# Kernel optimization log

Hardware: AMD Instinct MI355X
Metric: run time of the kernel (lower is better)

## Reference

```python
import jax, jax.numpy as jnp
import numpy as np

L = 6          # number of GNN layers
D = 128        # feature_dim (d_model)
H = 4          # num_heads (hardcoded in AttentionalPropagation)
DH = D // H    # per-head dim
N = 2048       # number of segments/keypoints per frame
B = 1          # batch
NAMES = ["self", "cross"] * (L // 2)
EPS = 1e-5     # InstanceNorm1d eps


def _conv1(W, b, x):
    # Conv1d kernel_size=1: W [out,in], x [b,in,n] -> [b,out,n]
    return jnp.einsum('oi,bin->bon', W, x) + b[None, :, None]


def _inorm(x):
    # InstanceNorm1d (affine=False): normalize over the length axis per (batch, channel)
    m = jnp.mean(x, axis=-1, keepdims=True)
    v = jnp.mean((x - m) ** 2, axis=-1, keepdims=True)
    return (x - m) * jax.lax.rsqrt(v + EPS)


def _attn_block(x, src, p):
    Wq, bq, Wk, bk, Wv, bv, Wm, bm, W1, b1, W2, b2 = p
    b_dim, _, n = x.shape
    # view(b, dim, heads, -1): channel axis split as (DH, H)
    q = _conv1(Wq, bq, x).reshape(b_dim, DH, H, -1)
    k = _conv1(Wk, bk, src).reshape(b_dim, DH, H, -1)
    v = _conv1(Wv, bv, src).reshape(b_dim, DH, H, -1)
    scores = jnp.einsum('bdhn,bdhm->bhnm', q, k) / jnp.sqrt(jnp.asarray(DH, x.dtype))
    prob = jax.nn.softmax(scores, axis=-1)
    msg = jnp.einsum('bhnm,bdhm->bdhn', prob, v).reshape(b_dim, D, -1)
    msg = _conv1(Wm, bm, msg)
    # MLP([2D, 2D, D]): Conv1d -> InstanceNorm1d -> ReLU -> Conv1d
    h = _conv1(W1, b1, jnp.concatenate([x, msg], axis=1))
    h = jax.nn.relu(_inorm(h))
    return _conv1(W2, b2, h)


def setup_inputs() -> dict:
    key = jax.random.key(0)
    ks = jax.random.split(key, 14)
    s = 0.05
    f32 = jnp.float32
    return {
        "desc0": jax.random.normal(ks[0], (B, D, N), f32),
        "desc1": jax.random.normal(ks[1], (B, D, N), f32),
        "Wq": jax.random.normal(ks[2], (L, D, D), f32) * s,
        "bq": jnp.zeros((L, D), f32),
        "Wk": jax.random.normal(ks[3], (L, D, D), f32) * s,
        "bk": jnp.zeros((L, D), f32),
        "Wv": jax.random.normal(ks[4], (L, D, D), f32) * s,
        "bv": jnp.zeros((L, D), f32),
        "Wm": jax.random.normal(ks[5], (L, D, D), f32) * s,
        "bm": jnp.zeros((L, D), f32),
        "W1": jax.random.normal(ks[6], (L, 2 * D, 2 * D), f32) * s,
        "b1": jnp.zeros((L, 2 * D), f32),
        "W2": jax.random.normal(ks[7], (L, D, 2 * D), f32) * s,
        "b2": jnp.zeros((L, D), f32),  # nn.init.constant_(mlp[-1].bias, 0.0)
    }


def reference(desc0, desc1, Wq, bq, Wk, bk, Wv, bv, Wm, bm, W1, b1, W2, b2):
    params = (Wq, bq, Wk, bk, Wv, bv, Wm, bm, W1, b1, W2, b2)
    for l in range(L):
        p = tuple(a[l] for a in params)
        if NAMES[l] == 'cross':
            src0, src1 = desc1, desc0
        else:
            src0, src1 = desc0, desc1
        delta0 = _attn_block(desc0, src0, p)
        delta1 = _attn_block(desc1, src1, p)
        desc0 = desc0 + delta0
        desc1 = desc1 + delta1
    return desc0, desc1
```

## Files before the change

kernel.cpp:

```cpp
#include <hip/hip_runtime.h>

#define NN 2048
#define DDIM 128
#define NHEAD 4
#define DH 32
#define NL 6

typedef __attribute__((ext_vector_type(8))) __bf16 bf16x8;
typedef __attribute__((ext_vector_type(4))) float f32x4;

__device__ __forceinline__ unsigned int f2bf(float x) {
  unsigned int u = __float_as_uint(x);
  u += 0x7fff + ((u >> 16) & 1);
  return u >> 16;
}
__device__ __forceinline__ unsigned int pk2(float a, float b) {
  return f2bf(a) | (f2bf(b) << 16);
}
__device__ __forceinline__ float bf2f(unsigned short u) {
  return __uint_as_float(((unsigned int)u) << 16);
}

__global__ __launch_bounds__(256) void setup_kernel(
    const float* __restrict__ Wq, const float* __restrict__ Wk,
    const float* __restrict__ Wv, const float* __restrict__ Wm,
    const float* __restrict__ W1, const float* __restrict__ W2,
    const float* __restrict__ bmv, const float* __restrict__ b1,
    const float* __restrict__ desc0, const float* __restrict__ desc1,
    unsigned short* __restrict__ Wqkv, unsigned short* __restrict__ Wb2,
    unsigned short* __restrict__ Wmix, float* __restrict__ b1m,
    unsigned short* __restrict__ dT0, unsigned short* __restrict__ dT1,
    float* __restrict__ o0, float* __restrict__ o1,
    float* __restrict__ SgAll) {
  __shared__ __align__(16) unsigned char ARENA[17408];
  const int bid = blockIdx.x;
  const int t = threadIdx.x;

  if (bid < 672) {
    int idx = (bid * 256 + t) * 4;
    if (idx >= 688128) return;
    const float* src; unsigned short* dst; int soff, doff;
    if (idx < 98304)       { src = Wq; soff = idx; dst = Wqkv; doff = idx; }
    else if (idx < 196608) { src = Wk; soff = idx - 98304; dst = Wqkv; doff = idx; }
    else if (idx < 294912) { src = Wv; soff = idx - 196608; dst = Wqkv; doff = idx; }
    else if (idx < 491520) { src = W2; soff = idx - 294912; dst = Wb2; doff = soff; }
    else {
      int f = idx - 491520;
      int l = f >> 15, rem = f & 32767;
      int i = rem >> 7, c = rem & 127;
      src = W1; soff = (l << 16) + (i << 8) + c;
      dst = Wmix; doff = (l << 16) + (i << 8) + c;
    }
    float4 v = *(const float4*)&src[soff];
    uint2 p = { pk2(v.x, v.y), pk2(v.z, v.w) };
    *(uint2*)&dst[doff] = p;
  } else if (bid < 720) {
    const int b = bid - 672;
    const int jb = b & 1, ib = (b >> 1) & 3, l = b >> 3;
    const int bj = jb * 64, bi = ib * 64;
    float* Ws = (float*)ARENA;
    float* Xs = (float*)ARENA + 2080;
    const int ti = (t >> 4) << 2;
    const int tj = (t & 15) << 2;
    float acc[4][4] = {{0.f}};
    for (int k0 = 0; k0 < 128; k0 += 32) {
#pragma unroll
      for (int i = 0; i < 8; ++i) {
        int e = t + i * 256;
        int ii = e >> 5, kk = e & 31;
        Ws[kk * 65 + ii] = W1[(size_t)(l << 16) + (bi + ii) * 256 + 128 + k0 + kk];
      }
#pragma unroll
      for (int i = 0; i < 2; ++i) {
        int e = t + i * 256;
        int r = e >> 4, c4 = e & 15;
        *(float4*)&Xs[r * 64 + c4 * 4] =
            *(const float4*)&Wm[(size_t)l * 16384 + (k0 + r) * 128 + bj + c4 * 4];
      }
      __syncthreads();
#pragma unroll
      for (int kk = 0; kk < 32; ++kk) {
        float a[4];
        a[0] = Ws[kk * 65 + ti]; a[1] = Ws[kk * 65 + ti + 1];
        a[2] = Ws[kk * 65 + ti + 2]; a[3] = Ws[kk * 65 + ti + 3];
        float4 b4 = *(const float4*)&Xs[kk * 64 + tj];
        float bb[4] = {b4.x, b4.y, b4.z, b4.w};
#pragma unroll
        for (int i = 0; i < 4; ++i)
#pragma unroll
          for (int j = 0; j < 4; ++j) acc[i][j] += a[i] * bb[j];
      }
      __syncthreads();
    }
#pragma unroll
    for (int i = 0; i < 4; ++i) {
      uint2 p = { pk2(acc[i][0], acc[i][1]), pk2(acc[i][2], acc[i][3]) };
      *(uint2*)&Wmix[(size_t)(l << 16) + (bi + ti + i) * 256 + 128 + bj + tj] = p;
    }
    if (jb == 0 && ib == 0) {
      float a = b1[l * 256 + t];
      const float* wr = &W1[(size_t)(l << 16) + t * 256 + 128];
      const float* bp = &bmv[l * 128];
      for (int k = 0; k < 128; k += 4)
        a += wr[k] * bp[k] + wr[k + 1] * bp[k + 1] + wr[k + 2] * bp[k + 2] + wr[k + 3] * bp[k + 3];
      b1m[l * 256 + t] = a;
    }
  } else if (bid < 784) {
    const int b = bid - 720;
    const float* D = (b >> 5) ? desc1 : desc0;
    unsigned short* T = (b >> 5) ? dT1 : dT0;
    float* O = (b >> 5) ? o1 : o0;
    const int n0 = (b & 31) * 64;
    unsigned short* L = (unsigned short*)ARENA;
#pragma unroll
    for (int i = 0; i < 8; ++i) {
      int idx = t + i * 256;
      int c = idx >> 4, nj = (idx & 15) * 4;
      float4 v = *(const float4*)&D[(size_t)c * NN + n0 + nj];
      *(float4*)&O[(size_t)c * NN + n0 + nj] = v;
      L[(nj + 0) * 136 + c] = (unsigned short)f2bf(v.x);
      L[(nj + 1) * 136 + c] = (unsigned short)f2bf(v.y);
      L[(nj + 2) * 136 + c] = (unsigned short)f2bf(v.z);
      L[(nj + 3) * 136 + c] = (unsigned short)f2bf(v.w);
    }
    __syncthreads();
#pragma unroll
    for (int i = 0; i < 4; ++i) {
      int idx = t + i * 256;
      int n = idx >> 4, cj = (idx & 15) * 8;
      uint4 v = *(const uint4*)&L[n * 136 + cj];
      *(uint4*)&T[(size_t)(n0 + n) * 128 + cj] = v;
    }
  } else {
    float4 z = make_float4(0.f, 0.f, 0.f, 0.f);
    *(float4*)&SgAll[(bid - 784) * 1024 + t * 4] = z;
  }
}

struct MOp {
  const unsigned short* A;
  const float* bias;
  const unsigned short* B1;
  const unsigned short* B2;
  unsigned short* Cb;
  float* Cf;
  const float* Sp;
  int ldb, ldc, mode;
};
struct MOps8 { MOp op[8]; };

template <int K>
__global__ __launch_bounds__(256) void gemm_direct_kernel(MOps8 P) {
  const MOp g = P.op[blockIdx.z];
  const int t = threadIdx.x;
  const int w = t >> 6, lane = t & 63;
  const int col = lane & 15, Qd = lane >> 4;
  const int bm = blockIdx.y * 64;
  const int bn = blockIdx.x * 64;

  __shared__ float meanL[256], rstdL[256];
  __shared__ float swS[4][64], swQ[4][64];

  if (g.mode == 4) {
    float s = g.Sp[t * 2], ss = g.Sp[t * 2 + 1];
    float mean = s * (1.0f / NN);
    float var = fmaxf(ss * (1.0f / NN) - mean * mean, 0.f);
    meanL[t] = mean;
    rstdL[t] = rsqrtf(var + 1e-5f);
  }
  __syncthreads();

  const int n = bn + w * 16 + col;
  f32x4 acc[4];
#pragma unroll
  for (int mt = 0; mt < 4; ++mt) acc[mt] = (f32x4){0.f, 0.f, 0.f, 0.f};

#pragma unroll
  for (int k0 = 0; k0 < K; k0 += 32) {
    bf16x8 af[4];
#pragma unroll
    for (int mt = 0; mt < 4; ++mt)
      af[mt] = *(const bf16x8*)&g.A[(size_t)(bm + mt * 16 + col) * K + k0 + Qd * 8];
    const unsigned short* Bp = g.B1;
    int kk = k0;
    if (g.B2 && k0 >= 128) { Bp = g.B2; kk = k0 - 128; }
    uint4 v = *(const uint4*)&Bp[(size_t)n * g.ldb + kk + Qd * 8];
    if (g.mode == 4) {
      float4 mA = *(const float4*)&meanL[k0 + Qd * 8];
      float4 mB = *(const float4*)&meanL[k0 + Qd * 8 + 4];
      float4 rA = *(const float4*)&rstdL[k0 + Qd * 8];
      float4 rB = *(const float4*)&rstdL[k0 + Qd * 8 + 4];
      union { uint4 q; unsigned short us[8]; } u;
      u.q = v;
      float x0 = fmaxf((bf2f(u.us[0]) - mA.x) * rA.x, 0.f);
      float x1 = fmaxf((bf2f(u.us[1]) - mA.y) * rA.y, 0.f);
      float x2 = fmaxf((bf2f(u.us[2]) - mA.z) * rA.z, 0.f);
      float x3 = fmaxf((bf2f(u.us[3]) - mA.w) * rA.w, 0.f);
      float x4 = fmaxf((bf2f(u.us[4]) - mB.x) * rB.x, 0.f);
      float x5 = fmaxf((bf2f(u.us[5]) - mB.y) * rB.y, 0.f);
      float x6 = fmaxf((bf2f(u.us[6]) - mB.z) * rB.z, 0.f);
      float x7 = fmaxf((bf2f(u.us[7]) - mB.w) * rB.w, 0.f);
      u.q.x = pk2(x0, x1); u.q.y = pk2(x2, x3);
      u.q.z = pk2(x4, x5); u.q.w = pk2(x6, x7);
      v = u.q;
    }
    union { uint4 q; bf16x8 b; } bc;
    bc.q = v;
#pragma unroll
    for (int mt = 0; mt < 4; ++mt)
      acc[mt] = __builtin_amdgcn_mfma_f32_16x16x32_bf16(af[mt], bc.b, acc[mt], 0, 0, 0);
  }

#pragma unroll
  for (int mt = 0; mt < 4; ++mt) {
    const int c0 = bm + mt * 16 + Qd * 4;
    const float b0 = g.bias[c0], b1 = g.bias[c0 + 1];
    const float b2 = g.bias[c0 + 2], b3 = g.bias[c0 + 3];
    f32x4 a = acc[mt];
    float v0 = a[0] + b0, v1 = a[1] + b1, v2 = a[2] + b2, v3 = a[3] + b3;
    if (g.mode <= 2) {
      if (g.mode == 0) {
        const float sc = 0.25503488f;
        v0 *= sc; v1 *= sc; v2 *= sc; v3 *= sc;
      }
      const int d = c0 >> 2;
      if (g.mode == 1) {
        g.Cb[((size_t)0 * NN + n) * 32 + d] = (unsigned short)f2bf(v0);
        g.Cb[((size_t)1 * NN + n) * 32 + d] = (unsigned short)f2bf(v1);
        g.Cb[((size_t)2 * NN + n) * 32 + d] = (unsigned short)f2bf(v2);
        g.Cb[((size_t)3 * NN + n) * 32 + d] = (unsigned short)f2bf(v3);
      } else {
        g.Cb[(size_t)(0 * 32 + d) * NN + n] = (unsigned short)f2bf(v0);
        g.Cb[(size_t)(1 * 32 + d) * NN + n] = (unsigned short)f2bf(v1);
        g.Cb[(size_t)(2 * 32 + d) * NN + n] = (unsigned short)f2bf(v2);
        g.Cb[(size_t)(3 * 32 + d) * NN + n] = (unsigned short)f2bf(v3);
      }
    } else if (g.mode == 5) {
      uint2 pv = { pk2(v0, v1), pk2(v2, v3) };
      *(uint2*)&g.Cb[(size_t)n * g.ldc + c0] = pv;
      float sA[4] = {v0, v1, v2, v3};
      float sQ[4] = {v0 * v0, v1 * v1, v2 * v2, v3 * v3};
#pragma unroll
      for (int r = 0; r < 4; ++r) {
#pragma unroll
        for (int off = 1; off < 16; off <<= 1) {
          sA[r] += __shfl_xor(sA[r], off);
          sQ[r] += __shfl_xor(sQ[r], off);
        }
      }
      if (col == 0) {
#pragma unroll
        for (int r = 0; r < 4; ++r) {
          swS[w][mt * 16 + Qd * 4 + r] = sA[r];
          swQ[w][mt * 16 + Qd * 4 + r] = sQ[r];
        }
      }
    } else {
      float* dp = g.Cf;
      float o0 = dp[(size_t)(c0 + 0) * NN + n] + v0;
      float o1 = dp[(size_t)(c0 + 1) * NN + n] + v1;
      float o2 = dp[(size_t)(c0 + 2) * NN + n] + v2;
      float o3 = dp[(size_t)(c0 + 3) * NN + n] + v3;
      dp[(size_t)(c0 + 0) * NN + n] = o0;
      dp[(size_t)(c0 + 1) * NN + n] = o1;
      dp[(size_t)(c0 + 2) * NN + n] = o2;
      dp[(size_t)(c0 + 3) * NN + n] = o3;
      uint2 pv = { pk2(o0, o1), pk2(o2, o3) };
      *(uint2*)&g.Cb[(size_t)n * g.ldc + c0] = pv;
    }
  }
  if (g.mode == 5) {
    __syncthreads();
    if (t < 64) {
      float a = swS[0][t] + swS[1][t] + swS[2][t] + swS[3][t];
      float b = swQ[0][t] + swQ[1][t] + swQ[2][t] + swQ[3][t];
      atomicAdd(&g.Cf[(bm + t) * 2], a);
      atomicAdd(&g.Cf[(bm + t) * 2 + 1], b);
    }
  }
}

struct FDesc {
  const unsigned short* HT; const float* Sp; float* outF; unsigned short* dT;
  unsigned short* Qb; unsigned short* Kt; unsigned short* Vb;
};
struct FArgs {
  FDesc d[2];
  const unsigned short *W2l, *Wql, *Wkl, *Wvl;
  const float *b2l, *bql, *bkl, *bvl;
};

__global__ __launch_bounds__(256) void fused_tail_kernel(FArgs F) {
  const FDesc g = F.d[blockIdx.y];
  const int t = threadIdx.x;
  const int w = t >> 6, lane = t & 63;
  const int col = lane & 15, Qd = lane >> 4;
  const int nb = blockIdx.x * 16;
  const int n = nb + col;

  __shared__ float meanL[256], rstdL[256];
  __shared__ __align__(16) unsigned short dTs[16 * 136];

  {
    float s = g.Sp[t * 2], ss = g.Sp[t * 2 + 1];
    float mean = s * (1.0f / NN);
    float var = fmaxf(ss * (1.0f / NN) - mean * mean, 0.f);
    meanL[t] = mean;
    rstdL[t] = rsqrtf(var + 1e-5f);
  }
  __syncthreads();

  f32x4 accA[2];
  accA[0] = (f32x4){0.f, 0.f, 0.f, 0.f};
  accA[1] = (f32x4){0.f, 0.f, 0.f, 0.f};
#pragma unroll
  for (int k0 = 0; k0 < 256; k0 += 32) {
    uint4 v = *(const uint4*)&g.HT[(size_t)n * 256 + k0 + Qd * 8];
    float4 mA = *(const float4*)&meanL[k0 + Qd * 8];
    float4 mB = *(const float4*)&meanL[k0 + Qd * 8 + 4];
    float4 rA = *(const float4*)&rstdL[k0 + Qd * 8];
    float4 rB = *(const float4*)&rstdL[k0 + Qd * 8 + 4];
    union { uint4 q; unsigned short us[8]; } u;
    u.q = v;
    float x0 = fmaxf((bf2f(u.us[0]) - mA.x) * rA.x, 0.f);
    float x1 = fmaxf((bf2f(u.us[1]) - mA.y) * rA.y, 0.f);
    float x2 = fmaxf((bf2f(u.us[2]) - mA.z) * rA.z, 0.f);
    float x3 = fmaxf((bf2f(u.us[3]) - mA.w) * rA.w, 0.f);
    float x4 = fmaxf((bf2f(u.us[4]) - mB.x) * rB.x, 0.f);
    float x5 = fmaxf((bf2f(u.us[5]) - mB.y) * rB.y, 0.f);
    float x6 = fmaxf((bf2f(u.us[6]) - mB.z) * rB.z, 0.f);
    float x7 = fmaxf((bf2f(u.us[7]) - mB.w) * rB.w, 0.f);
    u.q.x = pk2(x0, x1); u.q.y = pk2(x2, x3);
    u.q.z = pk2(x4, x5); u.q.w = pk2(x6, x7);
    union { uint4 q; bf16x8 b; } bc;
    bc.q = u.q;
#pragma unroll
    for (int mt = 0; mt < 2; ++mt) {
      bf16x8 af = *(const bf16x8*)&F.W2l[(size_t)(w * 32 + mt * 16 + col) * 256 + k0 + Qd * 8];
      accA[mt] = __builtin_amdgcn_mfma_f32_16x16x32_bf16(af, bc.b, accA[mt], 0, 0, 0);
    }
  }
#pragma unroll
  for (int mt = 0; mt < 2; ++mt) {
    const int c0 = w * 32 + mt * 16 + Qd * 4;
    f32x4 a = accA[mt];
    float o0 = g.outF[(size_t)(c0 + 0) * NN + n] + a[0] + F.b2l[c0 + 0];
    float o1 = g.outF[(size_t)(c0 + 1) * NN + n] + a[1] + F.b2l[c0 + 1];
    float o2 = g.outF[(size_t)(c0 + 2) * NN + n] + a[2] + F.b2l[c0 + 2];
    float o3 = g.outF[(size_t)(c0 + 3) * NN + n] + a[3] + F.b2l[c0 + 3];
    g.outF[(size_t)(c0 + 0) * NN + n] = o0;
    g.outF[(size_t)(c0 + 1) * NN + n] = o1;
    g.outF[(size_t)(c0 + 2) * NN + n] = o2;
    g.outF[(size_t)(c0 + 3) * NN + n] = o3;
    unsigned short s0 = (unsigned short)f2bf(o0), s1 = (unsigned short)f2bf(o1);
    unsigned short s2 = (unsigned short)f2bf(o2), s3 = (unsigned short)f2bf(o3);
    dTs[col * 136 + c0 + 0] = s0;
    dTs[col * 136 + c0 + 1] = s1;
    dTs[col * 136 + c0 + 2] = s2;
    dTs[col * 136 + c0 + 3] = s3;
    uint2 pv = { ((unsigned int)s0) | (((unsigned int)s1) << 16),
                 ((unsigned int)s2) | (((unsigned int)s3) << 16) };
    *(uint2*)&g.dT[(size_t)n * 128 + c0] = pv;
  }
  __syncthreads();

  f32x4 accB[6];
#pragma unroll
  for (int f = 0; f < 6; ++f) accB[f] = (f32x4){0.f, 0.f, 0.f, 0.f};
#pragma unroll
  for (int k0 = 0; k0 < 128; k0 += 32) {
    bf16x8 bq = *(const bf16x8*)&dTs[col * 136 + k0 + Qd * 8];
#pragma unroll
    for (int f = 0; f < 6; ++f) {
      const int idx = w * 6 + f;
      const int op = idx >> 3, mt = idx & 7;
      const unsigned short* W = (op == 0) ? F.Wql : (op == 1) ? F.Wkl : F.Wvl;
      bf16x8 af = *(const bf16x8*)&W[(size_t)(mt * 16 + col) * 128 + k0 + Qd * 8];
      accB[f] = __builtin_amdgcn_mfma_f32_16x16x32_bf16(af, bq, accB[f], 0, 0, 0);
    }
  }
#pragma unroll
  for (int f = 0; f < 6; ++f) {
    const int idx = w * 6 + f;
    const int op = idx >> 3, mt = idx & 7;
    const float* bias = (op == 0) ? F.bql : (op == 1) ? F.bkl : F.bvl;
    const int c0 = mt * 16 + Qd * 4;
    f32x4 a = accB[f];
    float v0 = a[0] + bias[c0], v1 = a[1] + bias[c0 + 1];
    float v2 = a[2] + bias[c0 + 2], v3 = a[3] + bias[c0 + 3];
    const int d = c0 >> 2;
    if (op == 0) {
      const float sc = 0.25503488f;
      v0 *= sc; v1 *= sc; v2 *= sc; v3 *= sc;
      g.Qb[(size_t)(0 * 32 + d) * NN + n] = (unsigned short)f2bf(v0);
      g.Qb[(size_t)(1 * 32 + d) * NN + n] = (unsigned short)f2bf(v1);
      g.Qb[(size_t)(2 * 32 + d) * NN + n] = (unsigned short)f2bf(v2);
      g.Qb[(size_t)(3 * 32 + d) * NN + n] = (unsigned short)f2bf(v3);
    } else if (op == 1) {
      g.Kt[((size_t)0 * NN + n) * 32 + d] = (unsigned short)f2bf(v0);
      g.Kt[((size_t)1 * NN + n) * 32 + d] = (unsigned short)f2bf(v1);
      g.Kt[((size_t)2 * NN + n) * 32 + d] = (unsigned short)f2bf(v2);
      g.Kt[((size_t)3 * NN + n) * 32 + d] = (unsigned short)f2bf(v3);
    } else {
      g.Vb[(size_t)(0 * 32 + d) * NN + n] = (unsigned short)f2bf(v0);
      g.Vb[(size_t)(1 * 32 + d) * NN + n] = (unsigned short)f2bf(v1);
      g.Vb[(size_t)(2 * 32 + d) * NN + n] = (unsigned short)f2bf(v2);
      g.Vb[(size_t)(3 * 32 + d) * NN + n] = (unsigned short)f2bf(v3);
    }
  }
}

__global__ __launch_bounds__(256, 4) void attn_mfma_kernel(
    const unsigned short* __restrict__ Qb0, const unsigned short* __restrict__ Kt0,
    const unsigned short* __restrict__ Vb0, const unsigned short* __restrict__ Qb1,
    const unsigned short* __restrict__ Kt1, const unsigned short* __restrict__ Vb1,
    unsigned short* __restrict__ mgT0, unsigned short* __restrict__ mgT1, int cross) {
  const int z = blockIdx.y, desc = z >> 2, h = z & 3;
  const int t = threadIdx.x;
  const int wid = t >> 6, lane = t & 63;
  const int col = lane & 15, Qd = lane >> 4;
  const int qb = blockIdx.x * 16;

  const unsigned short* Qb = desc ? Qb1 : Qb0;
  const int s = cross ? (1 - desc) : desc;
  const unsigned short* Kt = s ? Kt1 : Kt0;
  const unsigned short* Vb = s ? Vb1 : Vb0;

  __shared__ __align__(16) unsigned short SM[7424];
  unsigned short* PW = SM + wid * 640;
  float* fS = (float*)(SM + 2560);

  bf16x8 bq;
  {
    union { unsigned short u[8]; bf16x8 v; } tmp;
#pragma unroll
    for (int j = 0; j < 8; ++j)
      tmp.u[j] = Qb[(size_t)(h * 32 + Qd * 8 + j) * NN + qb + col];
    bq = tmp.v;
  }

  f32x4 o0 = {0.f, 0.f, 0.f, 0.f}, o1 = {0.f, 0.f, 0.f, 0.f};
  float m = -1e30f, l = 0.f;

  const int kq = wid * 512;
#pragma unroll 2
  for (int it = 0; it < 16; ++it) {
    const int k0 = kq + it * 32;
    bf16x8 aK0 = *(const bf16x8*)&Kt[((size_t)h * NN + k0 + col) * 32 + Qd * 8];
    bf16x8 aK1 = *(const bf16x8*)&Kt[((size_t)h * NN + k0 + 16 + col) * 32 + Qd * 8];
    bf16x8 av0 = *(const bf16x8*)&Vb[(size_t)(h * 32 + col) * NN + k0 + Qd * 8];
    bf16x8 av1 = *(const bf16x8*)&Vb[(size_t)(h * 32 + 16 + col) * NN + k0 + Qd * 8];
    f32x4 z4 = {0.f, 0.f, 0.f, 0.f};
    f32x4 s0 = __builtin_amdgcn_mfma_f32_16x16x32_bf16(aK0, bq, z4, 0, 0, 0);
    f32x4 s1 = __builtin_amdgcn_mfma_f32_16x16x32_bf16(aK1, bq, z4, 0, 0, 0);
    float cm = fmaxf(fmaxf(fmaxf(s0[0], s0[1]), fmaxf(s0[2], s0[3])),
                     fmaxf(fmaxf(s1[0], s1[1]), fmaxf(s1[2], s1[3])));
    cm = fmaxf(cm, __shfl_xor(cm, 16));
    cm = fmaxf(cm, __shfl_xor(cm, 32));
    const float mn = fmaxf(m, cm);
    const float alpha = exp2f(m - mn);
    m = mn;
    float p00 = exp2f(s0[0] - mn), p01 = exp2f(s0[1] - mn);
    float p02 = exp2f(s0[2] - mn), p03 = exp2f(s0[3] - mn);
    float p10 = exp2f(s1[0] - mn), p11 = exp2f(s1[1] - mn);
    float p12 = exp2f(s1[2] - mn), p13 = exp2f(s1[3] - mn);
    float us = (p00 + p01) + (p02 + p03) + (p10 + p11) + (p12 + p13);
    us += __shfl_xor(us, 16);
    us += __shfl_xor(us, 32);
    l = l * alpha + us;
    uint2 w0 = { pk2(p00, p01), pk2(p02, p03) };
    uint2 w1 = { pk2(p10, p11), pk2(p12, p13) };
    *(uint2*)&PW[col * 40 + Qd * 4] = w0;
    *(uint2*)&PW[col * 40 + 16 + Qd * 4] = w1;
    bf16x8 pb = *(const bf16x8*)&PW[col * 40 + Qd * 8];
    o0 = o0 * alpha;
    o1 = o1 * alpha;
    o0 = __builtin_amdgcn_mfma_f32_16x16x32_bf16(av0, pb, o0, 0, 0, 0);
    o1 = __builtin_amdgcn_mfma_f32_16x16x32_bf16(av1, pb, o1, 0, 0, 0);
  }

  __syncthreads();
  *(float4*)&fS[wid * 576 + col * 36 + Qd * 4] =
      make_float4(o0[0], o0[1], o0[2], o0[3]);
  *(float4*)&fS[wid * 576 + col * 36 + 16 + Qd * 4] =
      make_float4(o1[0], o1[1], o1[2], o1[3]);
  if (Qd == 0) {
    fS[2304 + wid * 16 + col] = m;
    fS[2368 + wid * 16 + col] = l;
  }
  __syncthreads();
  {
    const int q16 = t >> 4, dg = t & 15;
    float m0 = fS[2304 + q16], m1 = fS[2304 + 16 + q16];
    float m2 = fS[2304 + 32 + q16], m3 = fS[2304 + 48 + q16];
    float M = fmaxf(fmaxf(m0, m1), fmaxf(m2, m3));
    float w0 = exp2f(m0 - M), w1 = exp2f(m1 - M);
    float w2 = exp2f(m2 - M), w3 = exp2f(m3 - M);
    float L = w0 * fS[2368 + q16] + w1 * fS[2368 + 16 + q16] +
              w2 * fS[2368 + 32 + q16] + w3 * fS[2368 + 48 + q16];
    float inv = 1.0f / L;
    unsigned short* T = desc ? mgT1 : mgT0;
    const int q = qb + q16;
#pragma unroll
    for (int r = 0; r < 2; ++r) {
      int d = dg * 2 + r;
      float v = (w0 * fS[0 * 576 + q16 * 36 + d] + w1 * fS[1 * 576 + q16 * 36 + d] +
                 w2 * fS[2 * 576 + q16 * 36 + d] + w3 * fS[3 * 576 + q16 * 36 + d]) * inv;
      T[(size_t)q * 128 + d * 4 + h] = (unsigned short)f2bf(v);
    }
  }
}

extern "C" void kernel_launch(void* const* d_in, const int* in_sizes, int n_in,
                              void* d_out, int out_size, void* d_ws, size_t ws_size,
                              hipStream_t stream) {
  const float* desc0 = (const float*)d_in[0];
  const float* desc1 = (const float*)d_in[1];
  const float* Wq = (const float*)d_in[2];
  const float* bq = (const float*)d_in[3];
  const float* Wk = (const float*)d_in[4];
  const float* bk = (const float*)d_in[5];
  const float* Wv = (const float*)d_in[6];
  const float* bv = (const float*)d_in[7];
  const float* Wm = (const float*)d_in[8];
  const float* bmv = (const float*)d_in[9];
  const float* W1 = (const float*)d_in[10];
  const float* b1 = (const float*)d_in[11];
  const float* W2 = (const float*)d_in[12];
  const float* b2 = (const float*)d_in[13];

  float* out0 = (float*)d_out;
  float* out1 = out0 + (size_t)DDIM * NN;

  float* fws = (float*)d_ws;
  float* SgAll = fws;
  float* b1m = SgAll + 6144;
  unsigned short* uws = (unsigned short*)(b1m + 1536);
  unsigned short* dT0 = uws;
  unsigned short* dT1 = uws + 1 * 262144;
  unsigned short* Qb0 = uws + 2 * 262144;
  unsigned short* Qb1 = uws + 3 * 262144;
  unsigned short* Kt0 = uws + 4 * 262144;
  unsigned short* Kt1 = uws + 5 * 262144;
  unsigned short* Vb0 = uws + 6 * 262144;
  unsigned short* Vb1 = uws + 7 * 262144;
  unsigned short* mgT0 = uws + 8 * 262144;
  unsigned short* mgT1 = uws + 9 * 262144;
  unsigned short* HT0 = uws + 10 * 262144;
  unsigned short* HT1 = HT0 + 524288;
  unsigned short* Wqkv = HT1 + 524288;
  unsigned short* Wb2 = Wqkv + 294912;
  unsigned short* Wmix = Wb2 + 196608;

  setup_kernel<<<790, 256, 0, stream>>>(Wq, Wk, Wv, Wm, W1, W2, bmv, b1,
                                        desc0, desc1, Wqkv, Wb2, Wmix, b1m,
                                        dT0, dT1, out0, out1, SgAll);

  {
    MOps8 Pq = {};
    Pq.op[0] = {Wqkv, bq, dT0, nullptr, Qb0, nullptr, nullptr, 128, 0, 0};
    Pq.op[1] = {Wqkv, bq, dT1, nullptr, Qb1, nullptr, nullptr, 128, 0, 0};
    Pq.op[2] = {Wqkv + 98304, bk, dT0, nullptr, Kt0, nullptr, nullptr, 128, 0, 1};
    Pq.op[3] = {Wqkv + 98304, bk, dT1, nullptr, Kt1, nullptr, nullptr, 128, 0, 1};
    Pq.op[4] = {Wqkv + 196608, bv, dT0, nullptr, Vb0, nullptr, nullptr, 128, 0, 2};
    Pq.op[5] = {Wqkv + 196608, bv, dT1, nullptr, Vb1, nullptr, nullptr, 128, 0, 2};
    gemm_direct_kernel<128><<<dim3(32, 2, 6), 256, 0, stream>>>(Pq);
  }

  for (int l = 0; l < NL; ++l) {
    const int cross = l & 1;
    const unsigned short* wmx = Wmix + l * 65536;
    const unsigned short* w2 = Wb2 + l * 32768;
    const float* b1p = b1m + (size_t)l * 256;
    const float* b2p = b2 + (size_t)l * 128;
    float* Sg0 = SgAll + l * 1024;
    float* Sg1 = Sg0 + 512;

    attn_mfma_kernel<<<dim3(128, 8), 256, 0, stream>>>(
        Qb0, Kt0, Vb0, Qb1, Kt1, Vb1, mgT0, mgT1, cross);

    MOps8 P1 = {};
    P1.op[0] = {wmx, b1p, dT0, mgT0, HT0, Sg0, nullptr, 128, 256, 5};
    P1.op[1] = {wmx, b1p, dT1, mgT1, HT1, Sg1, nullptr, 128, 256, 5};
    gemm_direct_kernel<256><<<dim3(32, 4, 2), 256, 0, stream>>>(P1);

    if (l < NL - 1) {
      FArgs F;
      F.d[0] = {HT0, Sg0, out0, dT0, Qb0, Kt0, Vb0};
      F.d[1] = {HT1, Sg1, out1, dT1, Qb1, Kt1, Vb1};
      F.W2l = w2;
      F.Wql = Wqkv + (l + 1) * 16384;
      F.Wkl = Wqkv + 98304 + (l + 1) * 16384;
      F.Wvl = Wqkv + 196608 + (l + 1) * 16384;
      F.b2l = b2p;
      F.bql = bq + (size_t)(l + 1) * 128;
      F.bkl = bk + (size_t)(l + 1) * 128;
      F.bvl = bv + (size_t)(l + 1) * 128;
      fused_tail_kernel<<<dim3(128, 2), 256, 0, stream>>>(F);
    } else {
      MOps8 P2 = {};
      P2.op[0] = {w2, b2p, HT0, nullptr, dT0, out0, Sg0, 256, 128, 4};
      P2.op[1] = {w2, b2p, HT1, nullptr, dT1, out1, Sg1, 256, 128, 4};
      gemm_direct_kernel<256><<<dim3(32, 2, 2), 256, 0, stream>>>(P2);
    }
  }
}
```

Before: 402.7 us.

## Fuse attention and first MLP GEMM via last-arriving-block counter

Merges the attention kernel and the first MLP conv GEMM into one kernel. Each of the four head blocks for a 16-query tile increments a per-tile atomic counter, and the last block to arrive computes the 256-channel MLP1 GEMM for that tile. It then writes HT and accumulates instance-norm statistics with global atomics. This removes one kernel launch per layer and the gap between the two kernels, at the cost of a threadfence, more global atomics, and extra GEMM work on the winning block.

```diff
diff --git a/kernel.cpp b/kernel.cpp
--- a/kernel.cpp
+++ b/kernel.cpp
@@ -31,7 +31,7 @@
     unsigned short* __restrict__ Wmix, float* __restrict__ b1m,
     unsigned short* __restrict__ dT0, unsigned short* __restrict__ dT1,
     float* __restrict__ o0, float* __restrict__ o1,
-    float* __restrict__ SgAll) {
+    float* __restrict__ SgAll, float* __restrict__ cntAll) {
   __shared__ __align__(16) unsigned char ARENA[17408];
   const int bid = blockIdx.x;
   const int t = threadIdx.x;
@@ -132,8 +132,10 @@
       *(uint4*)&T[(size_t)(n0 + n) * 128 + cj] = v;
     }
   } else {
+    const int b = bid - 784;
     float4 z = make_float4(0.f, 0.f, 0.f, 0.f);
-    *(float4*)&SgAll[(bid - 784) * 1024 + t * 4] = z;
+    *(float4*)&SgAll[b * 1024 + t * 4] = z;
+    if (t < 64) *(float4*)&cntAll[b * 256 + t * 4] = z;
   }
 }
 
@@ -159,7 +161,6 @@
   const int bn = blockIdx.x * 64;
 
   __shared__ float meanL[256], rstdL[256];
-  __shared__ float swS[4][64], swQ[4][64];
 
   if (g.mode == 4) {
     float s = g.Sp[t * 2], ss = g.Sp[t * 2 + 1];
@@ -235,26 +236,6 @@
         g.Cb[(size_t)(2 * 32 + d) * NN + n] = (unsigned short)f2bf(v2);
         g.Cb[(size_t)(3 * 32 + d) * NN + n] = (unsigned short)f2bf(v3);
       }
-    } else if (g.mode == 5) {
-      uint2 pv = { pk2(v0, v1), pk2(v2, v3) };
-      *(uint2*)&g.Cb[(size_t)n * g.ldc + c0] = pv;
-      float sA[4] = {v0, v1, v2, v3};
-      float sQ[4] = {v0 * v0, v1 * v1, v2 * v2, v3 * v3};
-#pragma unroll
-      for (int r = 0; r < 4; ++r) {
-#pragma unroll
-        for (int off = 1; off < 16; off <<= 1) {
-          sA[r] += __shfl_xor(sA[r], off);
-          sQ[r] += __shfl_xor(sQ[r], off);
-        }
-      }
-      if (col == 0) {
-#pragma unroll
-        for (int r = 0; r < 4; ++r) {
-          swS[w][mt * 16 + Qd * 4 + r] = sA[r];
-          swQ[w][mt * 16 + Qd * 4 + r] = sQ[r];
-        }
-      }
     } else {
       float* dp = g.Cf;
       float o0 = dp[(size_t)(c0 + 0) * NN + n] + v0;
@@ -269,164 +250,34 @@
       *(uint2*)&g.Cb[(size_t)n * g.ldc + c0] = pv;
     }
   }
-  if (g.mode == 5) {
-    __syncthreads();
-    if (t < 64) {
-      float a = swS[0][t] + swS[1][t] + swS[2][t] + swS[3][t];
-      float b = swQ[0][t] + swQ[1][t] + swQ[2][t] + swQ[3][t];
-      atomicAdd(&g.Cf[(bm + t) * 2], a);
-      atomicAdd(&g.Cf[(bm + t) * 2 + 1], b);
-    }
-  }
-}
-
-struct FDesc {
-  const unsigned short* HT; const float* Sp; float* outF; unsigned short* dT;
-  unsigned short* Qb; unsigned short* Kt; unsigned short* Vb;
+}
+
+struct AArgs {
+  const unsigned short *Qb0, *Kt0, *Vb0, *Qb1, *Kt1, *Vb1;
+  unsigned short *mgT0, *mgT1;
+  const unsigned short *dT0, *dT1;
+  unsigned short *HT0, *HT1;
+  float *Sg0, *Sg1;
+  const unsigned short* Wmx;
+  const float* b1p;
+  int* cnt;
+  int cross;
 };
-struct FArgs {
-  FDesc d[2];
-  const unsigned short *W2l, *Wql, *Wkl, *Wvl;
-  const float *b2l, *bql, *bkl, *bvl;
-};
-
-__global__ __launch_bounds__(256) void fused_tail_kernel(FArgs F) {
-  const FDesc g = F.d[blockIdx.y];
-  const int t = threadIdx.x;
-  const int w = t >> 6, lane = t & 63;
-  const int col = lane & 15, Qd = lane >> 4;
-  const int nb = blockIdx.x * 16;
-  const int n = nb + col;
-
-  __shared__ float meanL[256], rstdL[256];
-  __shared__ __align__(16) unsigned short dTs[16 * 136];
-
-  {
-    float s = g.Sp[t * 2], ss = g.Sp[t * 2 + 1];
-    float mean = s * (1.0f / NN);
-    float var = fmaxf(ss * (1.0f / NN) - mean * mean, 0.f);
-    meanL[t] = mean;
-    rstdL[t] = rsqrtf(var + 1e-5f);
-  }
-  __syncthreads();
-
-  f32x4 accA[2];
-  accA[0] = (f32x4){0.f, 0.f, 0.f, 0.f};
-  accA[1] = (f32x4){0.f, 0.f, 0.f, 0.f};
-#pragma unroll
-  for (int k0 = 0; k0 < 256; k0 += 32) {
-    uint4 v = *(const uint4*)&g.HT[(size_t)n * 256 + k0 + Qd * 8];
-    float4 mA = *(const float4*)&meanL[k0 + Qd * 8];
-    float4 mB = *(const float4*)&meanL[k0 + Qd * 8 + 4];
-    float4 rA = *(const float4*)&rstdL[k0 + Qd * 8];
-    float4 rB = *(const float4*)&rstdL[k0 + Qd * 8 + 4];
-    union { uint4 q; unsigned short us[8]; } u;
-    u.q = v;
-    float x0 = fmaxf((bf2f(u.us[0]) - mA.x) * rA.x, 0.f);
-    float x1 = fmaxf((bf2f(u.us[1]) - mA.y) * rA.y, 0.f);
-    float x2 = fmaxf((bf2f(u.us[2]) - mA.z) * rA.z, 0.f);
-    float x3 = fmaxf((bf2f(u.us[3]) - mA.w) * rA.w, 0.f);
-    float x4 = fmaxf((bf2f(u.us[4]) - mB.x) * rB.x, 0.f);
-    float x5 = fmaxf((bf2f(u.us[5]) - mB.y) * rB.y, 0.f);
-    float x6 = fmaxf((bf2f(u.us[6]) - mB.z) * rB.z, 0.f);
-    float x7 = fmaxf((bf2f(u.us[7]) - mB.w) * rB.w, 0.f);
-    u.q.x = pk2(x0, x1); u.q.y = pk2(x2, x3);
-    u.q.z = pk2(x4, x5); u.q.w = pk2(x6, x7);
-    union { uint4 q; bf16x8 b; } bc;
-    bc.q = u.q;
-#pragma unroll
-    for (int mt = 0; mt < 2; ++mt) {
-      bf16x8 af = *(const bf16x8*)&F.W2l[(size_t)(w * 32 + mt * 16 + col) * 256 + k0 + Qd * 8];
-      accA[mt] = __builtin_amdgcn_mfma_f32_16x16x32_bf16(af, bc.b, accA[mt], 0, 0, 0);
-    }
-  }
-#pragma unroll
-  for (int mt = 0; mt < 2; ++mt) {
-    const int c0 = w * 32 + mt * 16 + Qd * 4;
-    f32x4 a = accA[mt];
-    float o0 = g.outF[(size_t)(c0 + 0) * NN + n] + a[0] + F.b2l[c0 + 0];
-    float o1 = g.outF[(size_t)(c0 + 1) * NN + n] + a[1] + F.b2l[c0 + 1];
-    float o2 = g.outF[(size_t)(c0 + 2) * NN + n] + a[2] + F.b2l[c0 + 2];
-    float o3 = g.outF[(size_t)(c0 + 3) * NN + n] + a[3] + F.b2l[c0 + 3];
-    g.outF[(size_t)(c0 + 0) * NN + n] = o0;
-    g.outF[(size_t)(c0 + 1) * NN + n] = o1;
-    g.outF[(size_t)(c0 + 2) * NN + n] = o2;
-    g.outF[(size_t)(c0 + 3) * NN + n] = o3;
-    unsigned short s0 = (unsigned short)f2bf(o0), s1 = (unsigned short)f2bf(o1);
-    unsigned short s2 = (unsigned short)f2bf(o2), s3 = (unsigned short)f2bf(o3);
-    dTs[col * 136 + c0 + 0] = s0;
-    dTs[col * 136 + c0 + 1] = s1;
-    dTs[col * 136 + c0 + 2] = s2;
-    dTs[col * 136 + c0 + 3] = s3;
-    uint2 pv = { ((unsigned int)s0) | (((unsigned int)s1) << 16),
-                 ((unsigned int)s2) | (((unsigned int)s3) << 16) };
-    *(uint2*)&g.dT[(size_t)n * 128 + c0] = pv;
-  }
-  __syncthreads();
-
-  f32x4 accB[6];
-#pragma unroll
-  for (int f = 0; f < 6; ++f) accB[f] = (f32x4){0.f, 0.f, 0.f, 0.f};
-#pragma unroll
-  for (int k0 = 0; k0 < 128; k0 += 32) {
-    bf16x8 bq = *(const bf16x8*)&dTs[col * 136 + k0 + Qd * 8];
-#pragma unroll
-    for (int f = 0; f < 6; ++f) {
-      const int idx = w * 6 + f;
-      const int op = idx >> 3, mt = idx & 7;
-      const unsigned short* W = (op == 0) ? F.Wql : (op == 1) ? F.Wkl : F.Wvl;
-      bf16x8 af = *(const bf16x8*)&W[(size_t)(mt * 16 + col) * 128 + k0 + Qd * 8];
-      accB[f] = __builtin_amdgcn_mfma_f32_16x16x32_bf16(af, bq, accB[f], 0, 0, 0);
-    }
-  }
-#pragma unroll
-  for (int f = 0; f < 6; ++f) {
-    const int idx = w * 6 + f;
-    const int op = idx >> 3, mt = idx & 7;
-    const float* bias = (op == 0) ? F.bql : (op == 1) ? F.bkl : F.bvl;
-    const int c0 = mt * 16 + Qd * 4;
-    f32x4 a = accB[f];
-    float v0 = a[0] + bias[c0], v1 = a[1] + bias[c0 + 1];
-    float v2 = a[2] + bias[c0 + 2], v3 = a[3] + bias[c0 + 3];
-    const int d = c0 >> 2;
-    if (op == 0) {
-      const float sc = 0.25503488f;
-      v0 *= sc; v1 *= sc; v2 *= sc; v3 *= sc;
-      g.Qb[(size_t)(0 * 32 + d) * NN + n] = (unsigned short)f2bf(v0);
-      g.Qb[(size_t)(1 * 32 + d) * NN + n] = (unsigned short)f2bf(v1);
-      g.Qb[(size_t)(2 * 32 + d) * NN + n] = (unsigned short)f2bf(v2);
-      g.Qb[(size_t)(3 * 32 + d) * NN + n] = (unsigned short)f2bf(v3);
-    } else if (op == 1) {
-      g.Kt[((size_t)0 * NN + n) * 32 + d] = (unsigned short)f2bf(v0);
-      g.Kt[((size_t)1 * NN + n) * 32 + d] = (unsigned short)f2bf(v1);
-      g.Kt[((size_t)2 * NN + n) * 32 + d] = (unsigned short)f2bf(v2);
-      g.Kt[((size_t)3 * NN + n) * 32 + d] = (unsigned short)f2bf(v3);
-    } else {
-      g.Vb[(size_t)(0 * 32 + d) * NN + n] = (unsigned short)f2bf(v0);
-      g.Vb[(size_t)(1 * 32 + d) * NN + n] = (unsigned short)f2bf(v1);
-      g.Vb[(size_t)(2 * 32 + d) * NN + n] = (unsigned short)f2bf(v2);
-      g.Vb[(size_t)(3 * 32 + d) * NN + n] = (unsigned short)f2bf(v3);
-    }
-  }
-}
-
-__global__ __launch_bounds__(256, 4) void attn_mfma_kernel(
-    const unsigned short* __restrict__ Qb0, const unsigned short* __restrict__ Kt0,
-    const unsigned short* __restrict__ Vb0, const unsigned short* __restrict__ Qb1,
-    const unsigned short* __restrict__ Kt1, const unsigned short* __restrict__ Vb1,
-    unsigned short* __restrict__ mgT0, unsigned short* __restrict__ mgT1, int cross) {
+
+__global__ __launch_bounds__(256, 4) void attn_mlp1_kernel(AArgs A) {
   const int z = blockIdx.y, desc = z >> 2, h = z & 3;
   const int t = threadIdx.x;
   const int wid = t >> 6, lane = t & 63;
   const int col = lane & 15, Qd = lane >> 4;
   const int qb = blockIdx.x * 16;
 
-  const unsigned short* Qb = desc ? Qb1 : Qb0;
-  const int s = cross ? (1 - desc) : desc;
-  const unsigned short* Kt = s ? Kt1 : Kt0;
-  const unsigned short* Vb = s ? Vb1 : Vb0;
+  const unsigned short* Qb = desc ? A.Qb1 : A.Qb0;
+  const int s = A.cross ? (1 - desc) : desc;
+  const unsigned short* Kt = s ? A.Kt1 : A.Kt0;
+  const unsigned short* Vb = s ? A.Vb1 : A.Vb0;
 
   __shared__ __align__(16) unsigned short SM[7424];
+  __shared__ int winflag;
   unsigned short* PW = SM + wid * 640;
   float* fS = (float*)(SM + 2560);
 
@@ -499,7 +350,7 @@
     float L = w0 * fS[2368 + q16] + w1 * fS[2368 + 16 + q16] +
               w2 * fS[2368 + 32 + q16] + w3 * fS[2368 + 48 + q16];
     float inv = 1.0f / L;
-    unsigned short* T = desc ? mgT1 : mgT0;
+    unsigned short* T = desc ? A.mgT1 : A.mgT0;
     const int q = qb + q16;
 #pragma unroll
     for (int r = 0; r < 2; ++r) {
@@ -507,6 +358,194 @@
       float v = (w0 * fS[0 * 576 + q16 * 36 + d] + w1 * fS[1 * 576 + q16 * 36 + d] +
                  w2 * fS[2 * 576 + q16 * 36 + d] + w3 * fS[3 * 576 + q16 * 36 + d]) * inv;
       T[(size_t)q * 128 + d * 4 + h] = (unsigned short)f2bf(v);
+    }
+  }
+
+  __threadfence();
+  __syncthreads();
+  if (t == 0) {
+    int old = atomicAdd(&A.cnt[desc * 128 + blockIdx.x], 1);
+    winflag = (old == 3) ? 1 : 0;
+  }
+  __syncthreads();
+  if (!winflag) return;
+  __threadfence();
+
+  const unsigned short* dT = desc ? A.dT1 : A.dT0;
+  const unsigned short* mgT = desc ? A.mgT1 : A.mgT0;
+  unsigned short* HT = desc ? A.HT1 : A.HT0;
+  float* Sg = desc ? A.Sg1 : A.Sg0;
+  const int n = qb + col;
+
+  f32x4 acc[4];
+#pragma unroll
+  for (int mt = 0; mt < 4; ++mt) acc[mt] = (f32x4){0.f, 0.f, 0.f, 0.f};
+#pragma unroll
+  for (int k0 = 0; k0 < 256; k0 += 32) {
+    const unsigned short* Bp = (k0 < 128) ? dT : mgT;
+    const int kk = k0 & 127;
+    union { uint4 q; bf16x8 b; } bc;
+    bc.q = *(const uint4*)&Bp[(size_t)n * 128 + kk + Qd * 8];
+#pragma unroll
+    for (int mt = 0; mt < 4; ++mt) {
+      bf16x8 af = *(const bf16x8*)&A.Wmx[(size_t)(wid * 64 + mt * 16 + col) * 256 + k0 + Qd * 8];
+      acc[mt] = __builtin_amdgcn_mfma_f32_16x16x32_bf16(af, bc.b, acc[mt], 0, 0, 0);
+    }
+  }
+#pragma unroll
+  for (int mt = 0; mt < 4; ++mt) {
+    const int c0 = wid * 64 + mt * 16 + Qd * 4;
+    f32x4 a = acc[mt];
+    float v0 = a[0] + A.b1p[c0], v1 = a[1] + A.b1p[c0 + 1];
+    float v2 = a[2] + A.b1p[c0 + 2], v3 = a[3] + A.b1p[c0 + 3];
+    uint2 pv = { pk2(v0, v1), pk2(v2, v3) };
+    *(uint2*)&HT[(size_t)n * 256 + c0] = pv;
+    float sA[4] = {v0, v1, v2, v3};
+    float sQ[4] = {v0 * v0, v1 * v1, v2 * v2, v3 * v3};
+#pragma unroll
+    for (int r = 0; r < 4; ++r) {
+#pragma unroll
+      for (int off = 1; off < 16; off <<= 1) {
+        sA[r] += __shfl_xor(sA[r], off);
+        sQ[r] += __shfl_xor(sQ[r], off);
+      }
+    }
+    if (col == 0) {
+#pragma unroll
+      for (int r = 0; r < 4; ++r) {
+        atomicAdd(&Sg[(c0 + r) * 2], sA[r]);
+        atomicAdd(&Sg[(c0 + r) * 2 + 1], sQ[r]);
+      }
+    }
+  }
+}
+
+struct FDesc {
+  const unsigned short* HT; const float* Sp; float* outF; unsigned short* dT;
+  unsigned short* Qb; unsigned short* Kt; unsigned short* Vb;
+};
+struct FArgs {
+  FDesc d[2];
+  const unsigned short *W2l, *Wql, *Wkl, *Wvl;
+  const float *b2l, *bql, *bkl, *bvl;
+};
+
+__global__ __launch_bounds__(256) void fused_tail_kernel(FArgs F) {
+  const FDesc g = F.d[blockIdx.y];
+  const int t = threadIdx.x;
+  const int w = t >> 6, lane = t & 63;
+  const int col = lane & 15, Qd = lane >> 4;
+  const int nb = blockIdx.x * 16;
+  const int n = nb + col;
+
+  __shared__ float meanL[256], rstdL[256];
+  __shared__ __align__(16) unsigned short dTs[16 * 136];
+
+  {
+    float s = g.Sp[t * 2], ss = g.Sp[t * 2 + 1];
+    float mean = s * (1.0f / NN);
+    float var = fmaxf(ss * (1.0f / NN) - mean * mean, 0.f);
+    meanL[t] = mean;
+    rstdL[t] = rsqrtf(var + 1e-5f);
+  }
+  __syncthreads();
+
+  f32x4 accA[2];
+  accA[0] = (f32x4){0.f, 0.f, 0.f, 0.f};
+  accA[1] = (f32x4){0.f, 0.f, 0.f, 0.f};
+#pragma unroll
+  for (int k0 = 0; k0 < 256; k0 += 32) {
+    uint4 v = *(const uint4*)&g.HT[(size_t)n * 256 + k0 + Qd * 8];
+    float4 mA = *(const float4*)&meanL[k0 + Qd * 8];
+    float4 mB = *(const float4*)&meanL[k0 + Qd * 8 + 4];
+    float4 rA = *(const float4*)&rstdL[k0 + Qd * 8];
+    float4 rB = *(const float4*)&rstdL[k0 + Qd * 8 + 4];
+    union { uint4 q; unsigned short us[8]; } u;
+    u.q = v;
+    float x0 = fmaxf((bf2f(u.us[0]) - mA.x) * rA.x, 0.f);
+    float x1 = fmaxf((bf2f(u.us[1]) - mA.y) * rA.y, 0.f);
+    float x2 = fmaxf((bf2f(u.us[2]) - mA.z) * rA.z, 0.f);
+    float x3 = fmaxf((bf2f(u.us[3]) - mA.w) * rA.w, 0.f);
+    float x4 = fmaxf((bf2f(u.us[4]) - mB.x) * rB.x, 0.f);
+    float x5 = fmaxf((bf2f(u.us[5]) - mB.y) * rB.y, 0.f);
+    float x6 = fmaxf((bf2f(u.us[6]) - mB.z) * rB.z, 0.f);
+    float x7 = fmaxf((bf2f(u.us[7]) - mB.w) * rB.w, 0.f);
+    u.q.x = pk2(x0, x1); u.q.y = pk2(x2, x3);
+    u.q.z = pk2(x4, x5); u.q.w = pk2(x6, x7);
+    union { uint4 q; bf16x8 b; } bc;
+    bc.q = u.q;
+#pragma unroll
+    for (int mt = 0; mt < 2; ++mt) {
+      bf16x8 af = *(const bf16x8*)&F.W2l[(size_t)(w * 32 + mt * 16 + col) * 256 + k0 + Qd * 8];
+      accA[mt] = __builtin_amdgcn_mfma_f32_16x16x32_bf16(af, bc.b, accA[mt], 0, 0, 0);
+    }
+  }
+#pragma unroll
+  for (int mt = 0; mt < 2; ++mt) {
+    const int c0 = w * 32 + mt * 16 + Qd * 4;
+    f32x4 a = accA[mt];
+    float o0 = g.outF[(size_t)(c0 + 0) * NN + n] + a[0] + F.b2l[c0 + 0];
+    float o1 = g.outF[(size_t)(c0 + 1) * NN + n] + a[1] + F.b2l[c0 + 1];
+    float o2 = g.outF[(size_t)(c0 + 2) * NN + n] + a[2] + F.b2l[c0 + 2];
+    float o3 = g.outF[(size_t)(c0 + 3) * NN + n] + a[3] + F.b2l[c0 + 3];
+    g.outF[(size_t)(c0 + 0) * NN + n] = o0;
+    g.outF[(size_t)(c0 + 1) * NN + n] = o1;
+    g.outF[(size_t)(c0 + 2) * NN + n] = o2;
+    g.outF[(size_t)(c0 + 3) * NN + n] = o3;
+    unsigned short s0 = (unsigned short)f2bf(o0), s1 = (unsigned short)f2bf(o1);
+    unsigned short s2 = (unsigned short)f2bf(o2), s3 = (unsigned short)f2bf(o3);
+    dTs[col * 136 + c0 + 0] = s0;
+    dTs[col * 136 + c0 + 1] = s1;
+    dTs[col * 136 + c0 + 2] = s2;
+    dTs[col * 136 + c0 + 3] = s3;
+    uint2 pv = { ((unsigned int)s0) | (((unsigned int)s1) << 16),
+                 ((unsigned int)s2) | (((unsigned int)s3) << 16) };
+    *(uint2*)&g.dT[(size_t)n * 128 + c0] = pv;
+  }
+  __syncthreads();
+
+  f32x4 accB[6];
+#pragma unroll
+  for (int f = 0; f < 6; ++f) accB[f] = (f32x4){0.f, 0.f, 0.f, 0.f};
+#pragma unroll
+  for (int k0 = 0; k0 < 128; k0 += 32) {
+    bf16x8 bq = *(const bf16x8*)&dTs[col * 136 + k0 + Qd * 8];
+#pragma unroll
+    for (int f = 0; f < 6; ++f) {
+      const int idx = w * 6 + f;
+      const int op = idx >> 3, mt = idx & 7;
+      const unsigned short* W = (op == 0) ? F.Wql : (op == 1) ? F.Wkl : F.Wvl;
+      bf16x8 af = *(const bf16x8*)&W[(size_t)(mt * 16 + col) * 128 + k0 + Qd * 8];
+      accB[f] = __builtin_amdgcn_mfma_f32_16x16x32_bf16(af, bq, accB[f], 0, 0, 0);
+    }
+  }
+#pragma unroll
+  for (int f = 0; f < 6; ++f) {
+    const int idx = w * 6 + f;
+    const int op = idx >> 3, mt = idx & 7;
+    const float* bias = (op == 0) ? F.bql : (op == 1) ? F.bkl : F.bvl;
+    const int c0 = mt * 16 + Qd * 4;
+    f32x4 a = accB[f];
+    float v0 = a[0] + bias[c0], v1 = a[1] + bias[c0 + 1];
+    float v2 = a[2] + bias[c0 + 2], v3 = a[3] + bias[c0 + 3];
+    const int d = c0 >> 2;
+    if (op == 0) {
+      const float sc = 0.25503488f;
+      v0 *= sc; v1 *= sc; v2 *= sc; v3 *= sc;
+      g.Qb[(size_t)(0 * 32 + d) * NN + n] = (unsigned short)f2bf(v0);
+      g.Qb[(size_t)(1 * 32 + d) * NN + n] = (unsigned short)f2bf(v1);
+      g.Qb[(size_t)(2 * 32 + d) * NN + n] = (unsigned short)f2bf(v2);
+      g.Qb[(size_t)(3 * 32 + d) * NN + n] = (unsigned short)f2bf(v3);
+    } else if (op == 1) {
+      g.Kt[((size_t)0 * NN + n) * 32 + d] = (unsigned short)f2bf(v0);
+      g.Kt[((size_t)1 * NN + n) * 32 + d] = (unsigned short)f2bf(v1);
+      g.Kt[((size_t)2 * NN + n) * 32 + d] = (unsigned short)f2bf(v2);
+      g.Kt[((size_t)3 * NN + n) * 32 + d] = (unsigned short)f2bf(v3);
+    } else {
+      g.Vb[(size_t)(0 * 32 + d) * NN + n] = (unsigned short)f2bf(v0);
+      g.Vb[(size_t)(1 * 32 + d) * NN + n] = (unsigned short)f2bf(v1);
+      g.Vb[(size_t)(2 * 32 + d) * NN + n] = (unsigned short)f2bf(v2);
+      g.Vb[(size_t)(3 * 32 + d) * NN + n] = (unsigned short)f2bf(v3);
     }
   }
 }
@@ -534,7 +573,8 @@
 
   float* fws = (float*)d_ws;
   float* SgAll = fws;
-  float* b1m = SgAll + 6144;
+  float* cntAll = SgAll + 6144;
+  float* b1m = cntAll + 1536;
   unsigned short* uws = (unsigned short*)(b1m + 1536);
   unsigned short* dT0 = uws;
   unsigned short* dT1 = uws + 1 * 262144;
@@ -554,7 +594,7 @@
 
   setup_kernel<<<790, 256, 0, stream>>>(Wq, Wk, Wv, Wm, W1, W2, bmv, b1,
                                         desc0, desc1, Wqkv, Wb2, Wmix, b1m,
-                                        dT0, dT1, out0, out1, SgAll);
+                                        dT0, dT1, out0, out1, SgAll, cntAll);
 
   {
     MOps8 Pq = {};
@@ -568,21 +608,23 @@
   }
 
   for (int l = 0; l < NL; ++l) {
-    const int cross = l & 1;
-    const unsigned short* wmx = Wmix + l * 65536;
     const unsigned short* w2 = Wb2 + l * 32768;
-    const float* b1p = b1m + (size_t)l * 256;
     const float* b2p = b2 + (size_t)l * 128;
     float* Sg0 = SgAll + l * 1024;
     float* Sg1 = Sg0 + 512;
 
-    attn_mfma_kernel<<<dim3(128, 8), 256, 0, stream>>>(
-        Qb0, Kt0, Vb0, Qb1, Kt1, Vb1, mgT0, mgT1, cross);
-
-    MOps8 P1 = {};
-    P1.op[0] = {wmx, b1p, dT0, mgT0, HT0, Sg0, nullptr, 128, 256, 5};
-    P1.op[1] = {wmx, b1p, dT1, mgT1, HT1, Sg1, nullptr, 128, 256, 5};
-    gemm_direct_kernel<256><<<dim3(32, 4, 2), 256, 0, stream>>>(P1);
+    AArgs A;
+    A.Qb0 = Qb0; A.Kt0 = Kt0; A.Vb0 = Vb0;
+    A.Qb1 = Qb1; A.Kt1 = Kt1; A.Vb1 = Vb1;
+    A.mgT0 = mgT0; A.mgT1 = mgT1;
+    A.dT0 = dT0; A.dT1 = dT1;
+    A.HT0 = HT0; A.HT1 = HT1;
+    A.Sg0 = Sg0; A.Sg1 = Sg1;
+    A.Wmx = Wmix + l * 65536;
+    A.b1p = b1m + (size_t)l * 256;
+    A.cnt = (int*)(cntAll + l * 256);
+    A.cross = l & 1;
+    attn_mlp1_kernel<<<dim3(128, 8), 256, 0, stream>>>(A);
 
     if (l < NL - 1) {
       FArgs F;
```

After: 1.203 ms. 199% more time.
